# Optimization experiments

Hardware: AMD Instinct MI355X
Metric: run time of the kernel (lower is better)

The kernel has to match this reference:

```python
import jax, jax.numpy as jnp
import numpy as np

KERNEL_SIZE = 3
DILATIONS = (1, 2, 3)


def setup_inputs() -> dict:
    key = jax.random.key(0)
    k0, k1, k2 = jax.random.split(key, 3)
    B, N, C = 16, 4096, 256
    x = jax.random.normal(k0, (B, N, C), jnp.float32)
    Wqkv = jax.random.normal(k1, (len(DILATIONS), C, 3 * C), jnp.float32) * 0.02
    Wproj = jax.random.normal(k2, (C, C), jnp.float32) * 0.02
    bproj = jnp.zeros((C,), jnp.float32)
    return {"x": x, "Wqkv": Wqkv, "Wproj": Wproj, "bproj": bproj}


def _window(t, dilation, ksize):
    """Gather dilated local windows along the token axis.
    t: (B, N, C) -> (B, N, ksize, C), zero-padded (matches nn.Unfold padding)."""
    B, N, C = t.shape
    pad = dilation * (ksize - 1) // 2
    tp = jnp.pad(t, ((0, 0), (pad, pad), (0, 0)))
    # idx[n, j] = n + j*dilation  indexes into the padded sequence
    idx = jnp.arange(N)[:, None] + jnp.arange(ksize)[None, :] * dilation  # (N, K)
    return tp[:, idx, :]  # (B, N, K, C)


def reference(x, Wqkv, Wproj, bproj):
    B, N, C = x.shape
    scale = C ** (-0.5)
    outs = []
    for i, d in enumerate(DILATIONS):
        qkv = x @ Wqkv[i]                      # (B, N, 3C)
        q, k, v = jnp.split(qkv, 3, axis=-1)   # each (B, N, C)
        kw = _window(k, d, KERNEL_SIZE)        # (B, N, K, C)
        vw = _window(v, d, KERNEL_SIZE)        # (B, N, K, C)
        logits = jnp.einsum('bnc,bnkc->bnk', q, kw) * scale
        attn = jax.nn.softmax(logits, axis=-1)  # (B, N, K)
        outs.append(jnp.einsum('bnk,bnkc->bnc', attn, vw))
    combined = jnp.mean(jnp.stack(outs, axis=0), axis=0)  # mean over dilation branches
    return combined @ Wproj + bproj
```

## Files before the change

### kernel.cpp

```cpp
#include <hip/hip_runtime.h>
#include <hip/hip_bf16.h>
#include <math.h>

#define BB 16
#define NN 4096
#define CC 256
#define NC 768
#define MTOT (BB * NN)

typedef __attribute__((ext_vector_type(8))) __bf16 bf16x8;
typedef __attribute__((ext_vector_type(4))) float f32x4;

__device__ __forceinline__ unsigned short f2bf(float f) {
    union { float f; unsigned int u; } v; v.f = f;
    unsigned int r = (v.u + 0x7FFFu + ((v.u >> 16) & 1u)) >> 16;
    return (unsigned short)r;
}
__device__ __forceinline__ float bf2f(unsigned short b) {
    union { unsigned int u; float f; } v; v.u = ((unsigned int)b) << 16;
    return v.f;
}

#define GL16(gp, lp) \
    __builtin_amdgcn_global_load_lds((const __attribute__((address_space(1))) void*)(gp), \
                                     (__attribute__((address_space(3))) void*)(lp), 16, 0, 0)

template<int KDIM>
__device__ __forceinline__ void gemm_tile(const unsigned short* __restrict__ A,
                                          const unsigned short* __restrict__ Bt,
                                          int bm, int bn,
                                          unsigned short* As, unsigned short* Bs,
                                          f32x4 (&acc)[4][4]) {
    const int tid = threadIdx.x;
    const int lane = tid & 63;
    const int wave = tid >> 6;
    const int q = lane >> 4;
    const int r16 = lane & 15;
    const int wm = (wave >> 1) * 64;
    const int wn = (wave & 1) * 64;

    const int e0 = tid, e1 = tid + 256;
    const int r0 = e0 >> 2, r1 = e1 >> 2;
    const int kc0 = (e0 & 3) ^ ((r0 >> 1) & 3);
    const int kc1 = (e1 & 3) ^ ((r1 >> 1) & 3);
    const unsigned short* gA0 = A + (size_t)(bm + r0) * KDIM + kc0 * 8;
    const unsigned short* gA1 = A + (size_t)(bm + r1) * KDIM + kc1 * 8;
    const unsigned short* gB0 = Bt + (size_t)(bn + r0) * KDIM + kc0 * 8;
    const unsigned short* gB1 = Bt + (size_t)(bn + r1) * KDIM + kc1 * 8;

    const int sw = (q ^ ((r16 >> 1) & 3)) * 8;

    for (int kt = 0; kt < KDIM; kt += 32) {
        if (kt) __syncthreads();
        GL16(gA0 + kt, As + e0 * 8);
        GL16(gA1 + kt, As + e1 * 8);
        GL16(gB0 + kt, Bs + e0 * 8);
        GL16(gB1 + kt, Bs + e1 * 8);
        __syncthreads();

        bf16x8 af[4], bfr[4];
#pragma unroll
        for (int mi = 0; mi < 4; ++mi)
            af[mi] = *(const bf16x8*)(As + (wm + mi * 16 + r16) * 32 + sw);
#pragma unroll
        for (int ni = 0; ni < 4; ++ni)
            bfr[ni] = *(const bf16x8*)(Bs + (wn + ni * 16 + r16) * 32 + sw);
#pragma unroll
        for (int mi = 0; mi < 4; ++mi)
#pragma unroll
            for (int ni = 0; ni < 4; ++ni)
                acc[mi][ni] = __builtin_amdgcn_mfma_f32_16x16x32_bf16(
                    af[mi], bfr[ni], acc[mi][ni], 0, 0, 0);
    }
}

__global__ __launch_bounds__(256) void conv_all(const float* __restrict__ Wqkv,
                                                const float* __restrict__ Wproj,
                                                unsigned short* __restrict__ Wqb,
                                                unsigned short* __restrict__ Wkb,
                                                unsigned short* __restrict__ Wvs,
                                                unsigned short* __restrict__ WpT) {
    int t = blockIdx.x * 256 + threadIdx.x;
    if (t < 3 * CC * NC) {
        unsigned short v = f2bf(Wqkv[t]);
        int ic = t / NC;
        int col = t - ic * NC;
        if (col < 256)       Wqb[(size_t)ic * CC + col] = v;
        else if (col < 512)  Wkb[(size_t)ic * CC + col - 256] = v;
        else                 Wvs[(size_t)ic * CC + col - 512] = v;
    } else {
        int e = t - 3 * CC * NC;
        int g = e >> 8, c = e & 255;
        WpT[e] = f2bf(Wproj[(size_t)c * CC + g]);
    }
}

__global__ __launch_bounds__(256) void wgemm(const unsigned short* __restrict__ Wqb,
                                             const unsigned short* __restrict__ Wkb,
                                             const unsigned short* __restrict__ Wvs,
                                             const unsigned short* __restrict__ WpT,
                                             unsigned short* __restrict__ MtY,
                                             unsigned short* __restrict__ PtZ) {
    const int z = blockIdx.z;
    const unsigned short *A, *Bt;
    unsigned short* C;
    int nout; float mult;
    if (z < 3) {
        if (blockIdx.x >= 2) return;
        A = Wkb + z * CC * CC; Bt = Wqb + z * CC * CC; C = MtY + z * CC * CC;
        nout = CC; mult = 0.0625f;
    } else {
        A = WpT; Bt = Wvs; C = PtZ;
        nout = NC; mult = 1.0f / 3.0f;
    }

    __shared__ unsigned short As[128 * 32];
    __shared__ unsigned short Bs[128 * 32];
    f32x4 acc[4][4];
#pragma unroll
    for (int i = 0; i < 4; ++i)
#pragma unroll
        for (int j = 0; j < 4; ++j) acc[i][j] = {0.f, 0.f, 0.f, 0.f};

    gemm_tile<CC>(A, Bt, blockIdx.y * 128, blockIdx.x * 128, As, Bs, acc);

    const int lane = threadIdx.x & 63;
    const int wave = threadIdx.x >> 6;
    const int q = lane >> 4, r16 = lane & 15;
    const int wm = (wave >> 1) * 64, wn = (wave & 1) * 64;
#pragma unroll
    for (int mi = 0; mi < 4; ++mi)
#pragma unroll
        for (int ni = 0; ni < 4; ++ni) {
            int row0 = blockIdx.y * 128 + wm + mi * 16 + q * 4;
            int col = blockIdx.x * 128 + wn + ni * 16 + r16;
#pragma unroll
            for (int r = 0; r < 4; ++r)
                C[(size_t)(row0 + r) * nout + col] = f2bf(acc[mi][ni][r] * mult);
        }
}

__global__ __launch_bounds__(256, 2) void mega(const float* __restrict__ xf,
                                               const unsigned short* __restrict__ MtY,
                                               const unsigned short* __restrict__ PtZ,
                                               const float* __restrict__ bias,
                                               float* __restrict__ out) {
    __shared__ __align__(16) unsigned short xbuf[70 * 264];
    __shared__ __align__(16) unsigned short bstage[2 * 8192];
    __shared__ __align__(16) unsigned short yseg[4 * 16 * 72];
    __shared__ __align__(16) float part[2][64][3];

    const int tid = threadIdx.x;
    const int lane = tid & 63;
    const int wv = tid >> 6;
    const int q = lane >> 4;
    const int r16 = lane & 15;
    const int tg = wv >> 1;
    const int cg = wv & 1;
    const int t0 = blockIdx.x * 64;
    const int tokb = tg * 32;

    const int c2t = tid >> 2;
    const int kct = (tid & 3) ^ ((tid >> 3) & 3);
    const unsigned short* mB = MtY + (size_t)c2t * CC + kct * 8;
    const unsigned short* pB = PtZ + (size_t)c2t * NC + kct * 8;

    auto issue_stage = [&](int gs) {
        if (gs >= 48) return;
        unsigned short* dst = bstage + (gs & 1) * 8192 + tid * 8;
        const int i2 = gs >> 4;
        const int r = gs & 15;
        if (r < 8) {
            const unsigned short* s0 =
                mB + (size_t)(i2 * 256 + (r >> 2) * 128) * CC + (r & 3) * 64;
            GL16(s0, dst);
            GL16(s0 + (size_t)64 * CC, dst + 2048);
            GL16(s0 + 32, dst + 4096);
            GL16(s0 + (size_t)64 * CC + 32, dst + 6144);
        } else {
            const unsigned short* s0 = pB + i2 * 256 + (r - 8) * 32;
            GL16(s0, dst);
            GL16(s0 + (size_t)64 * NC, dst + 2048);
            GL16(s0 + (size_t)128 * NC, dst + 4096);
            GL16(s0 + (size_t)192 * NC, dst + 6144);
        }
    };

    issue_stage(0);

    for (int it = 0; it < 9; ++it) {
        int e = it * 256 + tid;
        if (e < 2240) {
            int rr = e >> 5, c = e & 31;
            int gr = t0 - 3 + rr;
            gr = gr < 0 ? 0 : (gr > MTOT - 1 ? MTOT - 1 : gr);
            const float* xp = xf + (size_t)gr * CC + c * 8;
            float4 a = *(const float4*)xp;
            float4 b = *(const float4*)(xp + 4);
            unsigned short p[8];
            p[0] = f2bf(a.x); p[1] = f2bf(a.y); p[2] = f2bf(a.z); p[3] = f2bf(a.w);
            p[4] = f2bf(b.x); p[5] = f2bf(b.y); p[6] = f2bf(b.z); p[7] = f2bf(b.w);
            *(float4*)(xbuf + rr * 264 + c * 8) = *(const float4*)p;
        }
    }
    __syncthreads();

    bf16x8 af[16];
#pragma unroll
    for (int tf = 0; tf < 2; ++tf)
#pragma unroll
        for (int kt = 0; kt < 8; ++kt)
            af[tf * 8 + kt] = *(const bf16x8*)(xbuf + (3 + tokb + tf * 16 + r16) * 264 +
                                               kt * 32 + q * 8);

    f32x4 oacc[16];
#pragma unroll
    for (int j = 0; j < 16; ++j) oacc[j] = {0.f, 0.f, 0.f, 0.f};

    const int fragsw = q ^ ((r16 >> 1) & 3);

#pragma unroll 1
    for (int i = 0; i < 3; ++i) {
        const int dil = i + 1;
        f32x4 yacc[8];
#pragma unroll
        for (int j = 0; j < 8; ++j) yacc[j] = {0.f, 0.f, 0.f, 0.f};
        float dg[2][3];
        float wgt[2][3];
        union ZA { unsigned int w[4]; bf16x8 v; };
        ZA za[2];

#pragma unroll
        for (int sl = 0; sl < 8; ++sl) {
            asm volatile("s_waitcnt vmcnt(0)" ::: "memory");
            __builtin_amdgcn_s_barrier();
            __builtin_amdgcn_sched_barrier(0);
            const unsigned short* bp = bstage + (sl & 1) * 8192;
            issue_stage(i * 16 + sl + 1);
#pragma unroll
            for (int h = 0; h < 2; ++h) {
                bf16x8 bfr[4];
#pragma unroll
                for (int cfl = 0; cfl < 4; ++cfl)
                    bfr[cfl] = *(const bf16x8*)(bp + h * 4096 +
                                   ((cg * 64 + cfl * 16 + r16) * 4 + fragsw) * 8);
                __builtin_amdgcn_s_setprio(1);
#pragma unroll
                for (int tf = 0; tf < 2; ++tf)
#pragma unroll
                    for (int cfl = 0; cfl < 4; ++cfl)
                        yacc[tf * 4 + cfl] = __builtin_amdgcn_mfma_f32_16x16x32_bf16(
                            af[tf * 8 + (sl & 3) * 2 + h], bfr[cfl],
                            yacc[tf * 4 + cfl], 0, 0, 0);
                __builtin_amdgcn_s_setprio(0);
            }
            if (sl == 3 || sl == 7) {
                const int hh = sl >> 2;
                unsigned short* ys = yseg + wv * (16 * 72);
#pragma unroll
                for (int tf = 0; tf < 2; ++tf) {
#pragma unroll
                    for (int cfl = 0; cfl < 4; ++cfl)
#pragma unroll
                        for (int rr = 0; rr < 4; ++rr)
                            ys[(q * 4 + rr) * 72 + cfl * 16 + r16] =
                                f2bf(yacc[tf * 4 + cfl][rr]);
                    asm volatile("s_waitcnt lgkmcnt(0)" ::: "memory");
                    __builtin_amdgcn_sched_barrier(0);
                    bf16x8 ya0 = *(const bf16x8*)(ys + r16 * 72 + q * 8);
                    bf16x8 ya1 = *(const bf16x8*)(ys + r16 * 72 + 32 + q * 8);
                    f32x4 lc[3];
#pragma unroll
                    for (int j = 0; j < 3; ++j) lc[j] = {0.f, 0.f, 0.f, 0.f};
#pragma unroll
                    for (int j = 0; j < 3; ++j) {
                        const unsigned short* xr =
                            xbuf + (3 + tokb + tf * 16 + r16 + (j - 1) * dil) * 264 +
                            hh * 128 + cg * 64 + q * 8;
                        lc[j] = __builtin_amdgcn_mfma_f32_16x16x32_bf16(
                            ya0, *(const bf16x8*)xr, lc[j], 0, 0, 0);
                        lc[j] = __builtin_amdgcn_mfma_f32_16x16x32_bf16(
                            ya1, *(const bf16x8*)(xr + 32), lc[j], 0, 0, 0);
                    }
                    if (q == (r16 >> 2)) {
                        const int rs = r16 & 3;
#pragma unroll
                        for (int j = 0; j < 3; ++j) {
                            float v = rs == 0 ? lc[j][0] : rs == 1 ? lc[j][1]
                                    : rs == 2 ? lc[j][2] : lc[j][3];
                            dg[tf][j] = hh == 0 ? v : dg[tf][j] + v;
                        }
                    }
                }
                if (hh == 0) {
#pragma unroll
                    for (int j = 0; j < 8; ++j) yacc[j] = {0.f, 0.f, 0.f, 0.f};
                } else {
                    if (q == (r16 >> 2)) {
#pragma unroll
                        for (int tf = 0; tf < 2; ++tf) {
                            float* pp = &part[cg][tokb + tf * 16 + r16][0];
                            pp[0] = dg[tf][0]; pp[1] = dg[tf][1]; pp[2] = dg[tf][2];
                        }
                    }
                    asm volatile("s_waitcnt lgkmcnt(0)" ::: "memory");
                }
            }
        }

#pragma unroll
        for (int sl = 0; sl < 8; ++sl) {
            asm volatile("s_waitcnt vmcnt(0)" ::: "memory");
            __builtin_amdgcn_s_barrier();
            __builtin_amdgcn_sched_barrier(0);
            const unsigned short* bp = bstage + (sl & 1) * 8192;
            issue_stage(i * 16 + 8 + sl + 1);
            if (sl == 0) {
#pragma unroll
                for (int tf = 0; tf < 2; ++tf) {
                    const int tok = tokb + tf * 16 + r16;
                    float l0 = part[0][tok][0] + part[1][tok][0];
                    float l1 = part[0][tok][1] + part[1][tok][1];
                    float l2 = part[0][tok][2] + part[1][tok][2];
                    const int ns = (t0 + tok) & (NN - 1);
                    const bool vlo = ns >= dil;
                    const bool vhi = ns + dil < NN;
                    l0 = vlo ? l0 : 0.f;
                    l2 = vhi ? l2 : 0.f;
                    float mx = fmaxf(l0, fmaxf(l1, l2));
                    float e0 = __expf(l0 - mx), e1 = __expf(l1 - mx), e2 = __expf(l2 - mx);
                    float inv = 1.0f / (e0 + e1 + e2);
                    wgt[tf][0] = vlo ? e0 * inv : 0.f;
                    wgt[tf][1] = e1 * inv;
                    wgt[tf][2] = vhi ? e2 * inv : 0.f;
                }
            }
#pragma unroll
            for (int tf = 0; tf < 2; ++tf) {
                const unsigned short* xr1 =
                    xbuf + (3 + tokb + tf * 16 + r16) * 264 + sl * 32 + q * 8;
                bf16x8 a0 = *(const bf16x8*)(xr1 - dil * 264);
                bf16x8 a2 = *(const bf16x8*)(xr1 + dil * 264);
                const unsigned short* u0 = (const unsigned short*)&a0;
                const unsigned short* u1 = (const unsigned short*)&af[tf * 8 + sl];
                const unsigned short* u2 = (const unsigned short*)&a2;
                const float w0 = wgt[tf][0], w1 = wgt[tf][1], w2 = wgt[tf][2];
#pragma unroll
                for (int e2i = 0; e2i < 4; ++e2i) {
                    float zl = w0 * bf2f(u0[e2i * 2]) + w1 * bf2f(u1[e2i * 2]) +
                               w2 * bf2f(u2[e2i * 2]);
                    float zh = w0 * bf2f(u0[e2i * 2 + 1]) + w1 * bf2f(u1[e2i * 2 + 1]) +
                               w2 * bf2f(u2[e2i * 2 + 1]);
                    asm("v_cvt_pk_bf16_f32 %0, %1, %2"
                        : "=v"(za[tf].w[e2i]) : "v"(zl), "v"(zh));
                }
            }
            __builtin_amdgcn_s_setprio(1);
#pragma unroll
            for (int ch = 0; ch < 2; ++ch)
#pragma unroll
                for (int cfl = 0; cfl < 4; ++cfl) {
                    bf16x8 b = *(const bf16x8*)(bp + (ch * 2 + cg) * 2048 +
                                    ((cfl * 16 + r16) * 4 + fragsw) * 8);
#pragma unroll
                    for (int tf = 0; tf < 2; ++tf)
                        oacc[tf * 8 + ch * 4 + cfl] =
                            __builtin_amdgcn_mfma_f32_16x16x32_bf16(
                                za[tf].v, b, oacc[tf * 8 + ch * 4 + cfl], 0, 0, 0);
                }
            __builtin_amdgcn_s_setprio(0);
        }
    }

#pragma unroll
    for (int tf = 0; tf < 2; ++tf)
#pragma unroll
        for (int cf = 0; cf < 8; ++cf) {
            const int gc = (cf >> 2) * 128 + cg * 64 + (cf & 3) * 16 + r16;
            float bc = bias[gc];
            f32x4 v = oacc[tf * 8 + cf];
#pragma unroll
            for (int r = 0; r < 4; ++r)
                out[(size_t)(t0 + tokb + tf * 16 + q * 4 + r) * CC + gc] = v[r] + bc;
        }
}

extern "C" void kernel_launch(void* const* d_in, const int* in_sizes, int n_in,
                              void* d_out, int out_size, void* d_ws, size_t ws_size,
                              hipStream_t stream) {
    const float* x = (const float*)d_in[0];
    const float* Wqkv = (const float*)d_in[1];
    const float* Wproj = (const float*)d_in[2];
    const float* bproj = (const float*)d_in[3];
    float* out = (float*)d_out;

    unsigned short* Wqb = (unsigned short*)d_ws;
    unsigned short* Wkb = Wqb + (size_t)3 * CC * CC;
    unsigned short* Wvs = Wkb + (size_t)3 * CC * CC;
    unsigned short* WpT = Wvs + (size_t)3 * CC * CC;
    unsigned short* MtY = WpT + (size_t)CC * CC;
    unsigned short* PtZ = MtY + (size_t)NC * CC;

    conv_all<<<(3 * CC * NC + CC * CC) / 256, 256, 0, stream>>>(
        Wqkv, Wproj, Wqb, Wkb, Wvs, WpT);
    wgemm<<<dim3(6, 2, 4), 256, 0, stream>>>(Wqb, Wkb, Wvs, WpT, MtY, PtZ);
    mega<<<MTOT / 64, 256, 0, stream>>>(x, MtY, PtZ, bproj, out);
}
```

Baseline: 200.0 us.

## Fuse weight conversion into prep GEMM and re-partition logit stage across waves

Replaces the separate fp32-to-bf16 weight conversion kernel and the weight GEMM with one prep kernel that loads fp32 weights, converts them and stages them into LDS directly, removing one launch and an intermediate buffer round trip. In the main kernel, the logit phase now gives each wave all 64 tokens and a 64-column slice of the Y product. This removes the two-half accumulation and needs four-way partial sums in shared memory. It costs more registers (32 A fragments, 16 accumulators), which may hurt occupancy, and the fp32 Wproj loads in prep are strided.

Measured after the change: 403.0 us. +101.5%, slower.

```diff
diff --git a/kernel.cpp b/kernel.cpp
--- a/kernel.cpp
+++ b/kernel.cpp
@@ -25,12 +25,20 @@
     __builtin_amdgcn_global_load_lds((const __attribute__((address_space(1))) void*)(gp), \
                                      (__attribute__((address_space(3))) void*)(lp), 16, 0, 0)
 
-template<int KDIM>
-__device__ __forceinline__ void gemm_tile(const unsigned short* __restrict__ A,
-                                          const unsigned short* __restrict__ Bt,
-                                          int bm, int bn,
-                                          unsigned short* As, unsigned short* Bs,
-                                          f32x4 (&acc)[4][4]) {
+__global__ __launch_bounds__(256) void prep(const float* __restrict__ Wqkv,
+                                            const float* __restrict__ Wproj,
+                                            unsigned short* __restrict__ MtY,
+                                            unsigned short* __restrict__ PtZ) {
+    const int z = blockIdx.z;
+    if (z < 3 && blockIdx.x >= 2) return;
+    const int bm = blockIdx.y * 128, bn = blockIdx.x * 128;
+    const int nout = (z < 3) ? CC : NC;
+    const float mult = (z < 3) ? 0.0625f : (1.0f / 3.0f);
+    unsigned short* C = (z < 3) ? (MtY + (size_t)z * CC * CC) : PtZ;
+
+    __shared__ unsigned short As[128 * 32];
+    __shared__ unsigned short Bs[128 * 32];
+
     const int tid = threadIdx.x;
     const int lane = tid & 63;
     const int wave = tid >> 6;
@@ -38,102 +46,88 @@
     const int r16 = lane & 15;
     const int wm = (wave >> 1) * 64;
     const int wn = (wave & 1) * 64;
-
-    const int e0 = tid, e1 = tid + 256;
-    const int r0 = e0 >> 2, r1 = e1 >> 2;
-    const int kc0 = (e0 & 3) ^ ((r0 >> 1) & 3);
-    const int kc1 = (e1 & 3) ^ ((r1 >> 1) & 3);
-    const unsigned short* gA0 = A + (size_t)(bm + r0) * KDIM + kc0 * 8;
-    const unsigned short* gA1 = A + (size_t)(bm + r1) * KDIM + kc1 * 8;
-    const unsigned short* gB0 = Bt + (size_t)(bn + r0) * KDIM + kc0 * 8;
-    const unsigned short* gB1 = Bt + (size_t)(bn + r1) * KDIM + kc1 * 8;
-
     const int sw = (q ^ ((r16 >> 1) & 3)) * 8;
 
-    for (int kt = 0; kt < KDIM; kt += 32) {
+    const int r0 = tid >> 2, kc0 = (tid & 3) ^ ((r0 >> 1) & 3);
+    const int e1 = tid + 256, r1 = e1 >> 2, kc1 = ((e1 & 3)) ^ ((r1 >> 1) & 3);
+
+    f32x4 acc[4][4];
+#pragma unroll
+    for (int i = 0; i < 4; ++i)
+#pragma unroll
+        for (int j = 0; j < 4; ++j) acc[i][j] = {0.f, 0.f, 0.f, 0.f};
+
+    for (int kt = 0; kt < CC; kt += 32) {
         if (kt) __syncthreads();
-        GL16(gA0 + kt, As + e0 * 8);
-        GL16(gA1 + kt, As + e1 * 8);
-        GL16(gB0 + kt, Bs + e0 * 8);
-        GL16(gB1 + kt, Bs + e1 * 8);
+        {
+            float v[8];
+            unsigned short p8[8];
+            if (z < 3) {
+                const float* p = Wqkv + (size_t)(z * 256 + bm + r0) * NC + 256 + kt + kc0 * 8;
+                float4 a = *(const float4*)p, b = *(const float4*)(p + 4);
+                v[0]=a.x; v[1]=a.y; v[2]=a.z; v[3]=a.w; v[4]=b.x; v[5]=b.y; v[6]=b.z; v[7]=b.w;
+            } else {
+                const float* p = Wproj + (size_t)(kt + kc0 * 8) * CC + bm + r0;
+#pragma unroll
+                for (int j = 0; j < 8; ++j) v[j] = p[(size_t)j * CC];
+            }
+#pragma unroll
+            for (int j = 0; j < 8; ++j) p8[j] = f2bf(v[j]);
+            *(float4*)(As + tid * 8) = *(const float4*)p8;
+            if (z < 3) {
+                const float* p = Wqkv + (size_t)(z * 256 + bm + r1) * NC + 256 + kt + kc1 * 8;
+                float4 a = *(const float4*)p, b = *(const float4*)(p + 4);
+                v[0]=a.x; v[1]=a.y; v[2]=a.z; v[3]=a.w; v[4]=b.x; v[5]=b.y; v[6]=b.z; v[7]=b.w;
+            } else {
+                const float* p = Wproj + (size_t)(kt + kc1 * 8) * CC + bm + r1;
+#pragma unroll
+                for (int j = 0; j < 8; ++j) v[j] = p[(size_t)j * CC];
+            }
+#pragma unroll
+            for (int j = 0; j < 8; ++j) p8[j] = f2bf(v[j]);
+            *(float4*)(As + e1 * 8) = *(const float4*)p8;
+            {
+                const float* p = (z < 3)
+                    ? Wqkv + (size_t)(z * 256 + bn + r0) * NC + kt + kc0 * 8
+                    : Wqkv + (size_t)(bn + r0) * NC + 512 + kt + kc0 * 8;
+                float4 a = *(const float4*)p, b = *(const float4*)(p + 4);
+                p8[0]=f2bf(a.x); p8[1]=f2bf(a.y); p8[2]=f2bf(a.z); p8[3]=f2bf(a.w);
+                p8[4]=f2bf(b.x); p8[5]=f2bf(b.y); p8[6]=f2bf(b.z); p8[7]=f2bf(b.w);
+                *(float4*)(Bs + tid * 8) = *(const float4*)p8;
+            }
+            {
+                const float* p = (z < 3)
+                    ? Wqkv + (size_t)(z * 256 + bn + r1) * NC + kt + kc1 * 8
+                    : Wqkv + (size_t)(bn + r1) * NC + 512 + kt + kc1 * 8;
+                float4 a = *(const float4*)p, b = *(const float4*)(p + 4);
+                p8[0]=f2bf(a.x); p8[1]=f2bf(a.y); p8[2]=f2bf(a.z); p8[3]=f2bf(a.w);
+                p8[4]=f2bf(b.x); p8[5]=f2bf(b.y); p8[6]=f2bf(b.z); p8[7]=f2bf(b.w);
+                *(float4*)(Bs + e1 * 8) = *(const float4*)p8;
+            }
+        }
         __syncthreads();
 
-        bf16x8 af[4], bfr[4];
+        bf16x8 afv[4], bfv[4];
 #pragma unroll
         for (int mi = 0; mi < 4; ++mi)
-            af[mi] = *(const bf16x8*)(As + (wm + mi * 16 + r16) * 32 + sw);
+            afv[mi] = *(const bf16x8*)(As + (wm + mi * 16 + r16) * 32 + sw);
 #pragma unroll
         for (int ni = 0; ni < 4; ++ni)
-            bfr[ni] = *(const bf16x8*)(Bs + (wn + ni * 16 + r16) * 32 + sw);
+            bfv[ni] = *(const bf16x8*)(Bs + (wn + ni * 16 + r16) * 32 + sw);
 #pragma unroll
         for (int mi = 0; mi < 4; ++mi)
 #pragma unroll
             for (int ni = 0; ni < 4; ++ni)
                 acc[mi][ni] = __builtin_amdgcn_mfma_f32_16x16x32_bf16(
-                    af[mi], bfr[ni], acc[mi][ni], 0, 0, 0);
+                    afv[mi], bfv[ni], acc[mi][ni], 0, 0, 0);
     }
-}
-
-__global__ __launch_bounds__(256) void conv_all(const float* __restrict__ Wqkv,
-                                                const float* __restrict__ Wproj,
-                                                unsigned short* __restrict__ Wqb,
-                                                unsigned short* __restrict__ Wkb,
-                                                unsigned short* __restrict__ Wvs,
-                                                unsigned short* __restrict__ WpT) {
-    int t = blockIdx.x * 256 + threadIdx.x;
-    if (t < 3 * CC * NC) {
-        unsigned short v = f2bf(Wqkv[t]);
-        int ic = t / NC;
-        int col = t - ic * NC;
-        if (col < 256)       Wqb[(size_t)ic * CC + col] = v;
-        else if (col < 512)  Wkb[(size_t)ic * CC + col - 256] = v;
-        else                 Wvs[(size_t)ic * CC + col - 512] = v;
-    } else {
-        int e = t - 3 * CC * NC;
-        int g = e >> 8, c = e & 255;
-        WpT[e] = f2bf(Wproj[(size_t)c * CC + g]);
-    }
-}
-
-__global__ __launch_bounds__(256) void wgemm(const unsigned short* __restrict__ Wqb,
-                                             const unsigned short* __restrict__ Wkb,
-                                             const unsigned short* __restrict__ Wvs,
-                                             const unsigned short* __restrict__ WpT,
-                                             unsigned short* __restrict__ MtY,
-                                             unsigned short* __restrict__ PtZ) {
-    const int z = blockIdx.z;
-    const unsigned short *A, *Bt;
-    unsigned short* C;
-    int nout; float mult;
-    if (z < 3) {
-        if (blockIdx.x >= 2) return;
-        A = Wkb + z * CC * CC; Bt = Wqb + z * CC * CC; C = MtY + z * CC * CC;
-        nout = CC; mult = 0.0625f;
-    } else {
-        A = WpT; Bt = Wvs; C = PtZ;
-        nout = NC; mult = 1.0f / 3.0f;
-    }
-
-    __shared__ unsigned short As[128 * 32];
-    __shared__ unsigned short Bs[128 * 32];
-    f32x4 acc[4][4];
-#pragma unroll
-    for (int i = 0; i < 4; ++i)
-#pragma unroll
-        for (int j = 0; j < 4; ++j) acc[i][j] = {0.f, 0.f, 0.f, 0.f};
-
-    gemm_tile<CC>(A, Bt, blockIdx.y * 128, blockIdx.x * 128, As, Bs, acc);
-
-    const int lane = threadIdx.x & 63;
-    const int wave = threadIdx.x >> 6;
-    const int q = lane >> 4, r16 = lane & 15;
-    const int wm = (wave >> 1) * 64, wn = (wave & 1) * 64;
+
 #pragma unroll
     for (int mi = 0; mi < 4; ++mi)
 #pragma unroll
         for (int ni = 0; ni < 4; ++ni) {
-            int row0 = blockIdx.y * 128 + wm + mi * 16 + q * 4;
-            int col = blockIdx.x * 128 + wn + ni * 16 + r16;
+            int row0 = bm + wm + mi * 16 + q * 4;
+            int col = bn + wn + ni * 16 + r16;
 #pragma unroll
             for (int r = 0; r < 4; ++r)
                 C[(size_t)(row0 + r) * nout + col] = f2bf(acc[mi][ni][r] * mult);
@@ -147,18 +141,17 @@
                                                float* __restrict__ out) {
     __shared__ __align__(16) unsigned short xbuf[70 * 264];
     __shared__ __align__(16) unsigned short bstage[2 * 8192];
-    __shared__ __align__(16) unsigned short yseg[4 * 16 * 72];
-    __shared__ __align__(16) float part[2][64][3];
+    __shared__ __align__(16) unsigned short yseg[4 * 16 * 66];
+    __shared__ __align__(16) float part[4][64][3];
 
     const int tid = threadIdx.x;
     const int lane = tid & 63;
     const int wv = tid >> 6;
     const int q = lane >> 4;
     const int r16 = lane & 15;
-    const int tg = wv >> 1;
+    const int t0 = blockIdx.x * 64;
+    const int tokb = (wv >> 1) * 32;
     const int cg = wv & 1;
-    const int t0 = blockIdx.x * 64;
-    const int tokb = tg * 32;
 
     const int c2t = tid >> 2;
     const int kct = (tid & 3) ^ ((tid >> 3) & 3);
@@ -171,12 +164,11 @@
         const int i2 = gs >> 4;
         const int r = gs & 15;
         if (r < 8) {
-            const unsigned short* s0 =
-                mB + (size_t)(i2 * 256 + (r >> 2) * 128) * CC + (r & 3) * 64;
+            const unsigned short* s0 = mB + (size_t)(i2 * 256) * CC + r * 32;
             GL16(s0, dst);
             GL16(s0 + (size_t)64 * CC, dst + 2048);
-            GL16(s0 + 32, dst + 4096);
-            GL16(s0 + (size_t)64 * CC + 32, dst + 6144);
+            GL16(s0 + (size_t)128 * CC, dst + 4096);
+            GL16(s0 + (size_t)192 * CC, dst + 6144);
         } else {
             const unsigned short* s0 = pB + i2 * 256 + (r - 8) * 32;
             GL16(s0, dst);
@@ -205,12 +197,12 @@
     }
     __syncthreads();
 
-    bf16x8 af[16];
-#pragma unroll
-    for (int tf = 0; tf < 2; ++tf)
+    bf16x8 af[32];
+#pragma unroll
+    for (int tf = 0; tf < 4; ++tf)
 #pragma unroll
         for (int kt = 0; kt < 8; ++kt)
-            af[tf * 8 + kt] = *(const bf16x8*)(xbuf + (3 + tokb + tf * 16 + r16) * 264 +
+            af[tf * 8 + kt] = *(const bf16x8*)(xbuf + (3 + tf * 16 + r16) * 264 +
                                                kt * 32 + q * 8);
 
     f32x4 oacc[16];
@@ -222,10 +214,9 @@
 #pragma unroll 1
     for (int i = 0; i < 3; ++i) {
         const int dil = i + 1;
-        f32x4 yacc[8];
-#pragma unroll
-        for (int j = 0; j < 8; ++j) yacc[j] = {0.f, 0.f, 0.f, 0.f};
-        float dg[2][3];
+        f32x4 yacc[16];
+#pragma unroll
+        for (int j = 0; j < 16; ++j) yacc[j] = {0.f, 0.f, 0.f, 0.f};
         float wgt[2][3];
         union ZA { unsigned int w[4]; bf16x8 v; };
         ZA za[2];
@@ -237,46 +228,42 @@
             __builtin_amdgcn_sched_barrier(0);
             const unsigned short* bp = bstage + (sl & 1) * 8192;
             issue_stage(i * 16 + sl + 1);
-#pragma unroll
-            for (int h = 0; h < 2; ++h) {
-                bf16x8 bfr[4];
+            bf16x8 bfr[4];
+#pragma unroll
+            for (int cfl = 0; cfl < 4; ++cfl)
+                bfr[cfl] = *(const bf16x8*)(bp + wv * 2048 +
+                               ((cfl * 16 + r16) * 4 + fragsw) * 8);
+            __builtin_amdgcn_s_setprio(1);
+#pragma unroll
+            for (int tf = 0; tf < 4; ++tf)
 #pragma unroll
                 for (int cfl = 0; cfl < 4; ++cfl)
-                    bfr[cfl] = *(const bf16x8*)(bp + h * 4096 +
-                                   ((cg * 64 + cfl * 16 + r16) * 4 + fragsw) * 8);
-                __builtin_amdgcn_s_setprio(1);
-#pragma unroll
-                for (int tf = 0; tf < 2; ++tf)
+                    yacc[tf * 4 + cfl] = __builtin_amdgcn_mfma_f32_16x16x32_bf16(
+                        af[tf * 8 + sl], bfr[cfl], yacc[tf * 4 + cfl], 0, 0, 0);
+            __builtin_amdgcn_s_setprio(0);
+
+            if (sl == 7) {
+                unsigned short* ys = yseg + wv * (16 * 66);
+#pragma unroll
+                for (int tf = 0; tf < 4; ++tf) {
 #pragma unroll
                     for (int cfl = 0; cfl < 4; ++cfl)
-                        yacc[tf * 4 + cfl] = __builtin_amdgcn_mfma_f32_16x16x32_bf16(
-                            af[tf * 8 + (sl & 3) * 2 + h], bfr[cfl],
-                            yacc[tf * 4 + cfl], 0, 0, 0);
-                __builtin_amdgcn_s_setprio(0);
-            }
-            if (sl == 3 || sl == 7) {
-                const int hh = sl >> 2;
-                unsigned short* ys = yseg + wv * (16 * 72);
-#pragma unroll
-                for (int tf = 0; tf < 2; ++tf) {
-#pragma unroll
-                    for (int cfl = 0; cfl < 4; ++cfl)
 #pragma unroll
                         for (int rr = 0; rr < 4; ++rr)
-                            ys[(q * 4 + rr) * 72 + cfl * 16 + r16] =
+                            ys[(q * 4 + rr) * 66 + cfl * 16 + r16] =
                                 f2bf(yacc[tf * 4 + cfl][rr]);
                     asm volatile("s_waitcnt lgkmcnt(0)" ::: "memory");
                     __builtin_amdgcn_sched_barrier(0);
-                    bf16x8 ya0 = *(const bf16x8*)(ys + r16 * 72 + q * 8);
-                    bf16x8 ya1 = *(const bf16x8*)(ys + r16 * 72 + 32 + q * 8);
+                    bf16x8 ya0 = *(const bf16x8*)(ys + r16 * 66 + q * 8);
+                    bf16x8 ya1 = *(const bf16x8*)(ys + r16 * 66 + 32 + q * 8);
                     f32x4 lc[3];
 #pragma unroll
                     for (int j = 0; j < 3; ++j) lc[j] = {0.f, 0.f, 0.f, 0.f};
 #pragma unroll
                     for (int j = 0; j < 3; ++j) {
                         const unsigned short* xr =
-                            xbuf + (3 + tokb + tf * 16 + r16 + (j - 1) * dil) * 264 +
-                            hh * 128 + cg * 64 + q * 8;
+                            xbuf + (3 + tf * 16 + r16 + (j - 1) * dil) * 264 +
+                            wv * 64 + q * 8;
                         lc[j] = __builtin_amdgcn_mfma_f32_16x16x32_bf16(
                             ya0, *(const bf16x8*)xr, lc[j], 0, 0, 0);
                         lc[j] = __builtin_amdgcn_mfma_f32_16x16x32_bf16(
@@ -288,23 +275,11 @@
                         for (int j = 0; j < 3; ++j) {
                             float v = rs == 0 ? lc[j][0] : rs == 1 ? lc[j][1]
                                     : rs == 2 ? lc[j][2] : lc[j][3];
-                            dg[tf][j] = hh == 0 ? v : dg[tf][j] + v;
+                            part[wv][tf * 16 + r16][j] = v;
                         }
                     }
                 }
-                if (hh == 0) {
-#pragma unroll
-                    for (int j = 0; j < 8; ++j) yacc[j] = {0.f, 0.f, 0.f, 0.f};
-                } else {
-                    if (q == (r16 >> 2)) {
-#pragma unroll
-                        for (int tf = 0; tf < 2; ++tf) {
-                            float* pp = &part[cg][tokb + tf * 16 + r16][0];
-                            pp[0] = dg[tf][0]; pp[1] = dg[tf][1]; pp[2] = dg[tf][2];
-                        }
-                    }
-                    asm volatile("s_waitcnt lgkmcnt(0)" ::: "memory");
-                }
+                asm volatile("s_waitcnt lgkmcnt(0)" ::: "memory");
             }
         }
 
@@ -317,11 +292,14 @@
             issue_stage(i * 16 + 8 + sl + 1);
             if (sl == 0) {
 #pragma unroll
-                for (int tf = 0; tf < 2; ++tf) {
-                    const int tok = tokb + tf * 16 + r16;
-                    float l0 = part[0][tok][0] + part[1][tok][0];
-                    float l1 = part[0][tok][1] + part[1][tok][1];
-                    float l2 = part[0][tok][2] + part[1][tok][2];
+                for (int tt = 0; tt < 2; ++tt) {
+                    const int tok = tokb + tt * 16 + r16;
+                    float l0 = part[0][tok][0] + part[1][tok][0] +
+                               part[2][tok][0] + part[3][tok][0];
+                    float l1 = part[0][tok][1] + part[1][tok][1] +
+                               part[2][tok][1] + part[3][tok][1];
+                    float l2 = part[0][tok][2] + part[1][tok][2] +
+                               part[2][tok][2] + part[3][tok][2];
                     const int ns = (t0 + tok) & (NN - 1);
                     const bool vlo = ns >= dil;
                     const bool vhi = ns + dil < NN;
@@ -330,21 +308,21 @@
                     float mx = fmaxf(l0, fmaxf(l1, l2));
                     float e0 = __expf(l0 - mx), e1 = __expf(l1 - mx), e2 = __expf(l2 - mx);
                     float inv = 1.0f / (e0 + e1 + e2);
-                    wgt[tf][0] = vlo ? e0 * inv : 0.f;
-                    wgt[tf][1] = e1 * inv;
-                    wgt[tf][2] = vhi ? e2 * inv : 0.f;
+                    wgt[tt][0] = vlo ? e0 * inv : 0.f;
+                    wgt[tt][1] = e1 * inv;
+                    wgt[tt][2] = vhi ? e2 * inv : 0.f;
                 }
             }
 #pragma unroll
-            for (int tf = 0; tf < 2; ++tf) {
+            for (int tt = 0; tt < 2; ++tt) {
                 const unsigned short* xr1 =
-                    xbuf + (3 + tokb + tf * 16 + r16) * 264 + sl * 32 + q * 8;
+                    xbuf + (3 + tokb + tt * 16 + r16) * 264 + sl * 32 + q * 8;
                 bf16x8 a0 = *(const bf16x8*)(xr1 - dil * 264);
                 bf16x8 a2 = *(const bf16x8*)(xr1 + dil * 264);
                 const unsigned short* u0 = (const unsigned short*)&a0;
-                const unsigned short* u1 = (const unsigned short*)&af[tf * 8 + sl];
+                const unsigned short* u1 = (const unsigned short*)&af[((wv >> 1) * 2 + tt) * 8 + sl];
                 const unsigned short* u2 = (const unsigned short*)&a2;
-                const float w0 = wgt[tf][0], w1 = wgt[tf][1], w2 = wgt[tf][2];
+                const float w0 = wgt[tt][0], w1 = wgt[tt][1], w2 = wgt[tt][2];
 #pragma unroll
                 for (int e2i = 0; e2i < 4; ++e2i) {
                     float zl = w0 * bf2f(u0[e2i * 2]) + w1 * bf2f(u1[e2i * 2]) +
@@ -352,7 +330,7 @@
                     float zh = w0 * bf2f(u0[e2i * 2 + 1]) + w1 * bf2f(u1[e2i * 2 + 1]) +
                                w2 * bf2f(u2[e2i * 2 + 1]);
                     asm("v_cvt_pk_bf16_f32 %0, %1, %2"
-                        : "=v"(za[tf].w[e2i]) : "v"(zl), "v"(zh));
+                        : "=v"(za[tt].w[e2i]) : "v"(zl), "v"(zh));
                 }
             }
             __builtin_amdgcn_s_setprio(1);
@@ -363,25 +341,25 @@
                     bf16x8 b = *(const bf16x8*)(bp + (ch * 2 + cg) * 2048 +
                                     ((cfl * 16 + r16) * 4 + fragsw) * 8);
 #pragma unroll
-                    for (int tf = 0; tf < 2; ++tf)
-                        oacc[tf * 8 + ch * 4 + cfl] =
+                    for (int tt = 0; tt < 2; ++tt)
+                        oacc[tt * 8 + ch * 4 + cfl] =
                             __builtin_amdgcn_mfma_f32_16x16x32_bf16(
-                                za[tf].v, b, oacc[tf * 8 + ch * 4 + cfl], 0, 0, 0);
+                                za[tt].v, b, oacc[tt * 8 + ch * 4 + cfl], 0, 0, 0);
                 }
             __builtin_amdgcn_s_setprio(0);
         }
     }
 
 #pragma unroll
-    for (int tf = 0; tf < 2; ++tf)
+    for (int tt = 0; tt < 2; ++tt)
 #pragma unroll
         for (int cf = 0; cf < 8; ++cf) {
             const int gc = (cf >> 2) * 128 + cg * 64 + (cf & 3) * 16 + r16;
             float bc = bias[gc];
-            f32x4 v = oacc[tf * 8 + cf];
+            f32x4 v = oacc[tt * 8 + cf];
 #pragma unroll
             for (int r = 0; r < 4; ++r)
-                out[(size_t)(t0 + tokb + tf * 16 + q * 4 + r) * CC + gc] = v[r] + bc;
+                out[(size_t)(t0 + tokb + tt * 16 + q * 4 + r) * CC + gc] = v[r] + bc;
         }
 }
 
@@ -394,15 +372,9 @@
     const float* bproj = (const float*)d_in[3];
     float* out = (float*)d_out;
 
-    unsigned short* Wqb = (unsigned short*)d_ws;
-    unsigned short* Wkb = Wqb + (size_t)3 * CC * CC;
-    unsigned short* Wvs = Wkb + (size_t)3 * CC * CC;
-    unsigned short* WpT = Wvs + (size_t)3 * CC * CC;
-    unsigned short* MtY = WpT + (size_t)CC * CC;
+    unsigned short* MtY = (unsigned short*)d_ws;
     unsigned short* PtZ = MtY + (size_t)NC * CC;
 
-    conv_all<<<(3 * CC * NC + CC * CC) / 256, 256, 0, stream>>>(
-        Wqkv, Wproj, Wqb, Wkb, Wvs, WpT);
-    wgemm<<<dim3(6, 2, 4), 256, 0, stream>>>(Wqb, Wkb, Wvs, WpT, MtY, PtZ);
+    prep<<<dim3(6, 2, 4), 256, 0, stream>>>(Wqkv, Wproj, MtY, PtZ);
     mega<<<MTOT / 64, 256, 0, stream>>>(x, MtY, PtZ, bproj, out);
 }
```
